# Kernel optimization log

Hardware: AMD Instinct MI355X
Metric: run time of the kernel (lower is better)

Reference implementation:

```python
import jax, jax.numpy as jnp
import numpy as np

B, T, D, E, C = 4, 4096, 2048, 8, 1024
H = D // E  # per-expert hidden = out_features // num_experts = 256


def setup_inputs() -> dict:
    key = jax.random.key(0)
    ks = jax.random.split(key, 7)
    x = jax.random.normal(ks[0], (B, T, D), dtype=jnp.float32)
    # nn.Linear-style init scale ~ 1/sqrt(fan_in)
    W1 = jax.random.normal(ks[1], (E, H, D), dtype=jnp.float32) / np.sqrt(D)
    b1 = jax.random.normal(ks[2], (E, H), dtype=jnp.float32) / np.sqrt(D)
    W2 = jax.random.normal(ks[3], (E, D, H), dtype=jnp.float32) / np.sqrt(D)
    b2 = jax.random.normal(ks[4], (D,), dtype=jnp.float32) / np.sqrt(D)
    expert_indices = jax.random.randint(ks[5], (B, E, C), 0, T, dtype=jnp.int32)
    expert_gate = jax.random.uniform(ks[6], (B, E, C), dtype=jnp.float32)
    return {"x": x, "W1": W1, "b1": b1, "W2": W2, "b2": b2,
            "expert_indices": expert_indices, "expert_gate": expert_gate,
            "num_tokens": T}


def reference(x, W1, b1, W2, b2, expert_indices, expert_gate, num_tokens):
    # x: (B,T,D); expert_indices/expert_gate: (B,E,C)
    Bb = x.shape[0]
    Ee, Cc = expert_indices.shape[1], expert_indices.shape[2]
    b_idx = jnp.arange(Bb)[:, None, None]
    # dispatch: gather tokens per expert -> (B,E,C,D)
    sel = x[b_idx, expert_indices]
    # contract: per-expert GEMM -> (B,E,C,H)
    h = jnp.einsum('becd,ehd->bech', sel, W1) + b1[None, :, None, :]
    h = jax.nn.gelu(h, approximate=False)
    # expand: per-expert GEMM -> (B,E,C,D), shared output bias
    y = jnp.einsum('bech,eoh->beco', h, W2) + b2
    y = y * expert_gate[..., None]
    # combine: gated scatter-add back to token positions -> (B,T,D)
    out = jnp.zeros((Bb, num_tokens, x.shape[2]), dtype=x.dtype)
    out = out.at[jnp.arange(Bb)[:, None], expert_indices.reshape(Bb, Ee * Cc)].add(
        y.reshape(Bb, Ee * Cc, -1))
    return out
```

## Files before the change

### kernel.cpp

```cpp
#include <hip/hip_runtime.h>
#include <hip/hip_bf16.h>
#include <math.h>

#define B_ 4
#define T_ 4096
#define D_ 2048
#define E_ 8
#define C_ 1024
#define H_ 256
#define SLOTCAP 32

typedef unsigned short u16;
typedef unsigned long long u64;
typedef __attribute__((ext_vector_type(8))) short short8;
typedef __attribute__((ext_vector_type(4))) float f32x4;

__device__ __forceinline__ u16 f2bf_n(float f) {
    union { __hip_bfloat16 b; u16 u; } v;
    v.b = __float2bfloat16(f);
    return v.u;
}
__device__ __forceinline__ float bf2f(u16 u) {
    union { unsigned u; float f; } v; v.u = ((unsigned)u) << 16;
    return v.f;
}

__device__ __forceinline__ int swz(int row, int chunk) {
    return (row << 6) + ((chunk ^ (row & 7)) << 3);
}

__device__ __forceinline__ void gload16(const void* g, void* l) {
    __builtin_amdgcn_global_load_lds(
        (const __attribute__((address_space(1))) void*)g,
        (__attribute__((address_space(3))) void*)l, 16, 0, 0);
}

__global__ __launch_bounds__(256) void conv_x_bf16(
    const float* __restrict__ src, u16* __restrict__ dst, int n)
{
    int i = (blockIdx.x * 256 + threadIdx.x) * 4;
    if (i >= n) return;
    f32x4 v = *reinterpret_cast<const f32x4*>(src + i);
    u16 o[4];
    o[0] = f2bf_n(v[0]); o[1] = f2bf_n(v[1]); o[2] = f2bf_n(v[2]); o[3] = f2bf_n(v[3]);
    *reinterpret_cast<u64*>(dst + i) = *reinterpret_cast<const u64*>(o);
}

__global__ __launch_bounds__(256) void conv_w1_img(
    const float* __restrict__ W1, u16* __restrict__ img)
{
    const int cid = blockIdx.x * 256 + threadIdx.x;
    const int e = cid >> 16;
    const int kt = (cid >> 11) & 31;
    const int row = (cid >> 3) & 255;
    const int sc = cid & 7;
    const float* s = W1 + (((size_t)e * 256 + row) * 2048 + kt * 64
                           + ((sc ^ (row & 7)) << 3));
    f32x4 v0 = *reinterpret_cast<const f32x4*>(s);
    f32x4 v1 = *reinterpret_cast<const f32x4*>(s + 4);
    u16 o[8];
    #pragma unroll
    for (int j = 0; j < 4; ++j) { o[j] = f2bf_n(v0[j]); o[j + 4] = f2bf_n(v1[j]); }
    *reinterpret_cast<short8*>(img + (size_t)cid * 8) =
        *reinterpret_cast<const short8*>(o);
}

__global__ __launch_bounds__(256) void conv_w2_img(
    const float* __restrict__ W2, u16* __restrict__ img)
{
    const int cid = blockIdx.x * 256 + threadIdx.x;
    const int e = cid >> 16;
    const int nt = (cid >> 13) & 7;
    const int kt = (cid >> 11) & 3;
    const int row = (cid >> 3) & 255;
    const int sc = cid & 7;
    const float* s = W2 + (((size_t)e * 2048 + nt * 256 + row) * 256 + kt * 64
                           + ((sc ^ (row & 7)) << 3));
    f32x4 v0 = *reinterpret_cast<const f32x4*>(s);
    f32x4 v1 = *reinterpret_cast<const f32x4*>(s + 4);
    u16 o[8];
    #pragma unroll
    for (int j = 0; j < 4; ++j) { o[j] = f2bf_n(v0[j]); o[j + 4] = f2bf_n(v1[j]); }
    *reinterpret_cast<short8*>(img + (size_t)cid * 8) =
        *reinterpret_cast<const short8*>(o);
}

__global__ __launch_bounds__(512) void gemm1_v8(
    const u16* __restrict__ xbf, const u16* __restrict__ W1img,
    const float* __restrict__ b1, const int* __restrict__ idx,
    u16* __restrict__ Himg)
{
    const int be = blockIdx.x;
    const int mt = blockIdx.y;
    const int b = be >> 3, e = be & 7;
    const int m0 = mt * 64;

    __shared__ __align__(16) u16 As[2][4096];
    __shared__ __align__(16) u16 Bs[2][16384];

    const int tid = threadIdx.x;
    const int lane = tid & 63, wid = tid >> 6;
    const int wm = wid >> 2, wn = wid & 3;
    const int l15 = lane & 15, lk = lane >> 4;

    const int row8 = tid >> 3, asc = tid & 7;
    const int tok = idx[(b * E_ + e) * C_ + m0 + row8];
    const u16* aSrc = xbf + ((size_t)b * T_ + tok) * D_
                          + ((asc ^ (row8 & 7)) << 3);
    const u16* bSrc = W1img + (size_t)e * 32 * 16384 + (size_t)tid * 8;
    const int wofs = wid * 512;

#define G1_ISSUE(buf, t)                                                      \
    do {                                                                      \
        gload16(aSrc + (t) * 64, &As[buf][wofs]);                             \
        const u16* b_ = bSrc + (size_t)(t) * 16384;                           \
        gload16(b_,         &Bs[buf][wofs]);                                  \
        gload16(b_ + 4096,  &Bs[buf][4096 + wofs]);                           \
        gload16(b_ + 8192,  &Bs[buf][8192 + wofs]);                           \
        gload16(b_ + 12288, &Bs[buf][12288 + wofs]);                          \
    } while (0)

    f32x4 acc[2][4];
    #pragma unroll
    for (int i = 0; i < 2; ++i)
        #pragma unroll
        for (int j = 0; j < 4; ++j)
            acc[i][j] = (f32x4){0.f, 0.f, 0.f, 0.f};

    G1_ISSUE(0, 0);
    G1_ISSUE(1, 1);

    const int NT = D_ / 64;
    for (int t = 0; t < NT; ++t) {
        const int cur = t & 1;
        if (t < NT - 1) asm volatile("s_waitcnt vmcnt(5)" ::: "memory");
        else            asm volatile("s_waitcnt vmcnt(0)" ::: "memory");
        __builtin_amdgcn_s_barrier();
        __builtin_amdgcn_sched_barrier(0);
        #pragma unroll
        for (int kk = 0; kk < 2; ++kk) {
            short8 af[2], bfr[4];
            #pragma unroll
            for (int m = 0; m < 2; ++m) {
                const int row = wm * 32 + m * 16 + l15;
                af[m] = *reinterpret_cast<const short8*>(
                    &As[cur][swz(row, kk * 4 + lk)]);
            }
            #pragma unroll
            for (int n = 0; n < 4; ++n) {
                const int row = wn * 64 + n * 16 + l15;
                bfr[n] = *reinterpret_cast<const short8*>(
                    &Bs[cur][swz(row, kk * 4 + lk)]);
            }
            __builtin_amdgcn_s_setprio(1);
            #pragma unroll
            for (int m = 0; m < 2; ++m)
                #pragma unroll
                for (int n = 0; n < 4; ++n)
                    acc[m][n] = __builtin_amdgcn_mfma_f32_16x16x32_bf16(
                        bfr[n], af[m], acc[m][n], 0, 0, 0);
            __builtin_amdgcn_s_setprio(0);
        }
        asm volatile("s_waitcnt lgkmcnt(0)" ::: "memory");
        __builtin_amdgcn_s_barrier();
        __builtin_amdgcn_sched_barrier(0);
        if (t + 2 < NT) G1_ISSUE(cur, t + 2);
    }
#undef G1_ISSUE

    const size_t hblk = ((size_t)(be * 16 + mt) * 4 + wn) * 4096;
    #pragma unroll
    for (int m = 0; m < 2; ++m) {
        const int row = wm * 32 + m * 16 + l15;
        #pragma unroll
        for (int n = 0; n < 4; ++n) {
            const int hb = wn * 64 + n * 16 + lk * 4;
            f32x4 bias = *reinterpret_cast<const f32x4*>(&b1[e * H_ + hb]);
            u16 o[4];
            #pragma unroll
            for (int r = 0; r < 4; ++r) {
                float h = acc[m][n][r] + bias[r];
                float g = 0.5f * h * (1.0f + erff(h * 0.70710678118f));
                o[r] = f2bf_n(g);
            }
            const int lc = (n * 2 + (lk >> 1)) ^ (row & 7);
            u16* p = Himg + hblk + row * 64 + lc * 8 + (lk & 1) * 4;
            *reinterpret_cast<u64*>(p) = *reinterpret_cast<const u64*>(o);
        }
    }
}

__global__ __launch_bounds__(512) void gemm2_v6(
    const u16* __restrict__ Himg, const u16* __restrict__ W2img,
    const float* __restrict__ b2, const float* __restrict__ gate,
    u16* __restrict__ Ybuf)
{
    const int be = blockIdx.x;
    const int yy = blockIdx.y;
    const int mt = yy >> 3, nt = yy & 7;
    const int b = be >> 3, e = be & 7;
    const int m0 = mt * 64, n0 = nt * 256;

    __shared__ __align__(16) u16 As[2][4096];
    __shared__ __align__(16) u16 Bs[2][16384];

    const int tid = threadIdx.x;
    const int lane = tid & 63, wid = tid >> 6;
    const int wm = wid >> 2, wn = wid & 3;
    const int l15 = lane & 15, lk = lane >> 4;

    const u16* aSrc = Himg + ((size_t)(be * 16 + mt) * 4) * 4096 + (size_t)tid * 8;
    const u16* bSrc = W2img + ((size_t)(e * 8 + nt) * 4) * 16384 + (size_t)tid * 8;
    const int wofs = wid * 512;

#define G2_ISSUE(buf, t)                                                      \
    do {                                                                      \
        gload16(aSrc + (size_t)(t) * 4096, &As[buf][wofs]);                   \
        const u16* b_ = bSrc + (size_t)(t) * 16384;                           \
        gload16(b_,         &Bs[buf][wofs]);                                  \
        gload16(b_ + 4096,  &Bs[buf][4096 + wofs]);                           \
        gload16(b_ + 8192,  &Bs[buf][8192 + wofs]);                           \
        gload16(b_ + 12288, &Bs[buf][12288 + wofs]);                          \
    } while (0)

    f32x4 acc[2][4];
    #pragma unroll
    for (int i = 0; i < 2; ++i)
        #pragma unroll
        for (int j = 0; j < 4; ++j)
            acc[i][j] = (f32x4){0.f, 0.f, 0.f, 0.f};

    G2_ISSUE(0, 0);
    G2_ISSUE(1, 1);

    const int NT = H_ / 64;
    for (int t = 0; t < NT; ++t) {
        const int cur = t & 1;
        if (t < NT - 1) asm volatile("s_waitcnt vmcnt(5)" ::: "memory");
        else            asm volatile("s_waitcnt vmcnt(0)" ::: "memory");
        __builtin_amdgcn_s_barrier();
        __builtin_amdgcn_sched_barrier(0);
        #pragma unroll
        for (int kk = 0; kk < 2; ++kk) {
            short8 af[2], bfr[4];
            #pragma unroll
            for (int m = 0; m < 2; ++m) {
                const int row = wm * 32 + m * 16 + l15;
                af[m] = *reinterpret_cast<const short8*>(
                    &As[cur][swz(row, kk * 4 + lk)]);
            }
            #pragma unroll
            for (int n = 0; n < 4; ++n) {
                const int row = wn * 64 + n * 16 + l15;
                bfr[n] = *reinterpret_cast<const short8*>(
                    &Bs[cur][swz(row, kk * 4 + lk)]);
            }
            __builtin_amdgcn_s_setprio(1);
            #pragma unroll
            for (int m = 0; m < 2; ++m)
                #pragma unroll
                for (int n = 0; n < 4; ++n)
                    acc[m][n] = __builtin_amdgcn_mfma_f32_16x16x32_bf16(
                        bfr[n], af[m], acc[m][n], 0, 0, 0);
            __builtin_amdgcn_s_setprio(0);
        }
        asm volatile("s_waitcnt lgkmcnt(0)" ::: "memory");
        __builtin_amdgcn_s_barrier();
        __builtin_amdgcn_sched_barrier(0);
        if (t + 2 < NT) G2_ISSUE(cur, t + 2);
    }
#undef G2_ISSUE

    const size_t ybase = (size_t)(b * E_ + e) * C_ + m0;
    #pragma unroll
    for (int m = 0; m < 2; ++m) {
        const int cl = wm * 32 + m * 16 + l15;
        const float g = gate[ybase + cl];
        u16* rowp = Ybuf + (ybase + cl) * (size_t)D_ + n0;
        #pragma unroll
        for (int n = 0; n < 4; ++n) {
            const int db = wn * 64 + n * 16 + lk * 4;
            f32x4 bias = *reinterpret_cast<const f32x4*>(&b2[n0 + db]);
            u16 o[4];
            #pragma unroll
            for (int r = 0; r < 4; ++r)
                o[r] = f2bf_n((acc[m][n][r] + bias[r]) * g);
            *reinterpret_cast<u64*>(rowp + db) = *reinterpret_cast<const u64*>(o);
        }
    }
}

__global__ __launch_bounds__(256) void fill_kernel(
    const int* __restrict__ idx, int* __restrict__ cnt,
    int* __restrict__ slots)
{
    int i = blockIdx.x * 256 + threadIdx.x;
    if (i >= B_ * E_ * C_) return;
    int b = i / (E_ * C_);
    int slot = i % (E_ * C_);
    int t = idx[i];
    int p = atomicAdd(&cnt[b * T_ + t], 1);
    if (p < SLOTCAP) slots[(b * T_ + t) * SLOTCAP + p] = slot;
}

__global__ __launch_bounds__(256) void combine_kernel(
    const u16* __restrict__ Ybuf, const int* __restrict__ cnt,
    const int* __restrict__ slots, float* __restrict__ out)
{
    const int bt = blockIdx.x;
    const int tid = threadIdx.x;
    __shared__ int sl[SLOTCAP];
    int n = cnt[bt];
    n = n > SLOTCAP ? SLOTCAP : n;
    if (tid < n) sl[tid] = slots[bt * SLOTCAP + tid];
    __syncthreads();
    const int b = bt >> 12;
    float a[8] = {0.f, 0.f, 0.f, 0.f, 0.f, 0.f, 0.f, 0.f};
    for (int s = 0; s < n; ++s) {
        const u16* yrow = Ybuf + ((size_t)b * (E_ * C_) + sl[s]) * D_ + tid * 8;
        short8 v = *reinterpret_cast<const short8*>(yrow);
        #pragma unroll
        for (int j = 0; j < 8; ++j) a[j] += bf2f((u16)v[j]);
    }
    float* orow = out + (size_t)bt * D_ + tid * 8;
    *reinterpret_cast<f32x4*>(orow)     = (f32x4){a[0], a[1], a[2], a[3]};
    *reinterpret_cast<f32x4*>(orow + 4) = (f32x4){a[4], a[5], a[6], a[7]};
}

extern "C" void kernel_launch(void* const* d_in, const int* in_sizes, int n_in,
                              void* d_out, int out_size, void* d_ws, size_t ws_size,
                              hipStream_t stream) {
    const float* x    = (const float*)d_in[0];
    const float* W1   = (const float*)d_in[1];
    const float* b1   = (const float*)d_in[2];
    const float* W2   = (const float*)d_in[3];
    const float* b2   = (const float*)d_in[4];
    const int*   idx  = (const int*)d_in[5];
    const float* gate = (const float*)d_in[6];
    float* out = (float*)d_out;

    const size_t nW = (size_t)E_ * H_ * D_;
    const size_t nX = (size_t)B_ * T_ * D_;
    const size_t nH = (size_t)B_ * E_ * C_ * H_;
    const size_t nY = (size_t)B_ * E_ * C_ * D_;

    u16* W1img = (u16*)d_ws;
    u16* W2img = W1img + nW;
    u16* Himg  = W2img + nW;
    u16* Ybuf  = Himg + nH;
    u16* xbf   = Ybuf;
    int* cnt   = (int*)(Ybuf + nY);
    int* slots = cnt + (size_t)B_ * T_;

    hipMemsetAsync(cnt, 0, (size_t)B_ * T_ * sizeof(int), stream);
    conv_w1_img<<<2048, 256, 0, stream>>>(W1, W1img);
    conv_w2_img<<<2048, 256, 0, stream>>>(W2, W2img);
    conv_x_bf16<<<(int)(nX / 1024), 256, 0, stream>>>(x, xbf, (int)nX);
    fill_kernel<<<(B_ * E_ * C_) / 256, 256, 0, stream>>>(idx, cnt, slots);

    gemm1_v8<<<dim3(32, 16), 512, 0, stream>>>(xbf, W1img, b1, idx, Himg);
    gemm2_v6<<<dim3(32, 128), 512, 0, stream>>>(Himg, W2img, b2, gate, Ybuf);
    combine_kernel<<<B_ * T_, 256, 0, stream>>>(Ybuf, cnt, slots, out);
}
```

Baseline: 223.9 us.

## Keep whole W2 panel resident in LDS and loop over M tiles per block

The second GEMM now loads the full 256x256 W2 panel for its expert/N-tile into shared memory once, then iterates over all 16 M tiles of H within one block, prefetching the next A tile during the epilogue. This removes the repeated reload of W2 tiles across 16 separate blocks and cuts the grid from 4096 to 256 blocks. In exchange it uses about 160KB of LDS per block, leaving one block per CU with single-buffered A, and the grid is 256 blocks, so latency hiding and parallelism are reduced.

```diff
diff --git a/kernel.cpp b/kernel.cpp
--- a/kernel.cpp
+++ b/kernel.cpp
@@ -190,104 +190,124 @@
     }
 }
 
-__global__ __launch_bounds__(512) void gemm2_v6(
+__global__ __launch_bounds__(512) void gemm2_v7(
     const u16* __restrict__ Himg, const u16* __restrict__ W2img,
     const float* __restrict__ b2, const float* __restrict__ gate,
     u16* __restrict__ Ybuf)
 {
     const int be = blockIdx.x;
-    const int yy = blockIdx.y;
-    const int mt = yy >> 3, nt = yy & 7;
+    const int nt = blockIdx.y;
     const int b = be >> 3, e = be & 7;
-    const int m0 = mt * 64, n0 = nt * 256;
-
-    __shared__ __align__(16) u16 As[2][4096];
-    __shared__ __align__(16) u16 Bs[2][16384];
+    const int n0 = nt * 256;
+
+    __shared__ __align__(16) u16 As[16384];
+    __shared__ __align__(16) u16 Bs[65536];
 
     const int tid = threadIdx.x;
     const int lane = tid & 63, wid = tid >> 6;
     const int wm = wid >> 2, wn = wid & 3;
     const int l15 = lane & 15, lk = lane >> 4;
-
-    const u16* aSrc = Himg + ((size_t)(be * 16 + mt) * 4) * 4096 + (size_t)tid * 8;
-    const u16* bSrc = W2img + ((size_t)(e * 8 + nt) * 4) * 16384 + (size_t)tid * 8;
     const int wofs = wid * 512;
 
-#define G2_ISSUE(buf, t)                                                      \
+    const u16* bPanel = W2img + (size_t)(e * 8 + nt) * 65536;
+    #pragma unroll
+    for (int j = 0; j < 16; ++j)
+        gload16(bPanel + (size_t)(j * 512 + tid) * 8, &Bs[j * 4096 + wofs]);
+
+    const u16* aBase = Himg + (size_t)(be * 16) * 16384 + (size_t)tid * 8;
+
+#define A_ISSUE(mt)                                                           \
     do {                                                                      \
-        gload16(aSrc + (size_t)(t) * 4096, &As[buf][wofs]);                   \
-        const u16* b_ = bSrc + (size_t)(t) * 16384;                           \
-        gload16(b_,         &Bs[buf][wofs]);                                  \
-        gload16(b_ + 4096,  &Bs[buf][4096 + wofs]);                           \
-        gload16(b_ + 8192,  &Bs[buf][8192 + wofs]);                           \
-        gload16(b_ + 12288, &Bs[buf][12288 + wofs]);                          \
+        const u16* a_ = aBase + (size_t)(mt) * 16384;                         \
+        gload16(a_,          &As[wofs]);                                      \
+        gload16(a_ + 4096,   &As[4096 + wofs]);                               \
+        gload16(a_ + 8192,   &As[8192 + wofs]);                               \
+        gload16(a_ + 12288,  &As[12288 + wofs]);                              \
     } while (0)
 
-    f32x4 acc[2][4];
-    #pragma unroll
-    for (int i = 0; i < 2; ++i)
-        #pragma unroll
-        for (int j = 0; j < 4; ++j)
-            acc[i][j] = (f32x4){0.f, 0.f, 0.f, 0.f};
-
-    G2_ISSUE(0, 0);
-    G2_ISSUE(1, 1);
-
-    const int NT = H_ / 64;
-    for (int t = 0; t < NT; ++t) {
-        const int cur = t & 1;
-        if (t < NT - 1) asm volatile("s_waitcnt vmcnt(5)" ::: "memory");
-        else            asm volatile("s_waitcnt vmcnt(0)" ::: "memory");
-        __builtin_amdgcn_s_barrier();
-        __builtin_amdgcn_sched_barrier(0);
-        #pragma unroll
-        for (int kk = 0; kk < 2; ++kk) {
-            short8 af[2], bfr[4];
-            #pragma unroll
-            for (int m = 0; m < 2; ++m) {
-                const int row = wm * 32 + m * 16 + l15;
-                af[m] = *reinterpret_cast<const short8*>(
-                    &As[cur][swz(row, kk * 4 + lk)]);
-            }
-            #pragma unroll
-            for (int n = 0; n < 4; ++n) {
-                const int row = wn * 64 + n * 16 + l15;
-                bfr[n] = *reinterpret_cast<const short8*>(
-                    &Bs[cur][swz(row, kk * 4 + lk)]);
-            }
-            __builtin_amdgcn_s_setprio(1);
-            #pragma unroll
-            for (int m = 0; m < 2; ++m)
-                #pragma unroll
-                for (int n = 0; n < 4; ++n)
-                    acc[m][n] = __builtin_amdgcn_mfma_f32_16x16x32_bf16(
-                        bfr[n], af[m], acc[m][n], 0, 0, 0);
-            __builtin_amdgcn_s_setprio(0);
-        }
+    A_ISSUE(0);
+
+    f32x4 bias[4];
+    #pragma unroll
+    for (int n = 0; n < 4; ++n)
+        bias[n] = *reinterpret_cast<const f32x4*>(
+            &b2[n0 + wn * 64 + n * 16 + lk * 4]);
+
+    const int gbase = (b * E_ + e) * C_;
+    const size_t ybase = (size_t)(b * E_ + e) * C_;
+
+    asm volatile("s_waitcnt vmcnt(0)" ::: "memory");
+    __builtin_amdgcn_s_barrier();
+    __builtin_amdgcn_sched_barrier(0);
+
+    for (int mt = 0; mt < 16; ++mt) {
+        f32x4 acc[2][4];
+        #pragma unroll
+        for (int i = 0; i < 2; ++i)
+            #pragma unroll
+            for (int j = 0; j < 4; ++j)
+                acc[i][j] = (f32x4){0.f, 0.f, 0.f, 0.f};
+
+        #pragma unroll
+        for (int t = 0; t < 4; ++t) {
+            #pragma unroll
+            for (int kk = 0; kk < 2; ++kk) {
+                short8 af[2], bfr[4];
+                #pragma unroll
+                for (int m = 0; m < 2; ++m) {
+                    const int row = wm * 32 + m * 16 + l15;
+                    af[m] = *reinterpret_cast<const short8*>(
+                        &As[t * 4096 + swz(row, kk * 4 + lk)]);
+                }
+                #pragma unroll
+                for (int n = 0; n < 4; ++n) {
+                    const int row = wn * 64 + n * 16 + l15;
+                    bfr[n] = *reinterpret_cast<const short8*>(
+                        &Bs[t * 16384 + swz(row, kk * 4 + lk)]);
+                }
+                __builtin_amdgcn_s_setprio(1);
+                #pragma unroll
+                for (int m = 0; m < 2; ++m)
+                    #pragma unroll
+                    for (int n = 0; n < 4; ++n)
+                        acc[m][n] = __builtin_amdgcn_mfma_f32_16x16x32_bf16(
+                            bfr[n], af[m], acc[m][n], 0, 0, 0);
+                __builtin_amdgcn_s_setprio(0);
+            }
+        }
+
         asm volatile("s_waitcnt lgkmcnt(0)" ::: "memory");
         __builtin_amdgcn_s_barrier();
         __builtin_amdgcn_sched_barrier(0);
-        if (t + 2 < NT) G2_ISSUE(cur, t + 2);
+
+        const float g0 = gate[gbase + mt * 64 + wm * 32 + l15];
+        const float g1 = gate[gbase + mt * 64 + wm * 32 + 16 + l15];
+        if (mt < 15) A_ISSUE(mt + 1);
+
+        #pragma unroll
+        for (int m = 0; m < 2; ++m) {
+            const int cl = wm * 32 + m * 16 + l15;
+            const float g = (m == 0) ? g0 : g1;
+            u16* rowp = Ybuf + (ybase + mt * 64 + cl) * (size_t)D_ + n0;
+            #pragma unroll
+            for (int n = 0; n < 4; ++n) {
+                const int db = wn * 64 + n * 16 + lk * 4;
+                u16 o[4];
+                #pragma unroll
+                for (int r = 0; r < 4; ++r)
+                    o[r] = f2bf_n((acc[m][n][r] + bias[n][r]) * g);
+                *reinterpret_cast<u64*>(rowp + db) =
+                    *reinterpret_cast<const u64*>(o);
+            }
+        }
+
+        if (mt < 15) {
+            asm volatile("s_waitcnt vmcnt(8)" ::: "memory");
+            __builtin_amdgcn_s_barrier();
+            __builtin_amdgcn_sched_barrier(0);
+        }
     }
-#undef G2_ISSUE
-
-    const size_t ybase = (size_t)(b * E_ + e) * C_ + m0;
-    #pragma unroll
-    for (int m = 0; m < 2; ++m) {
-        const int cl = wm * 32 + m * 16 + l15;
-        const float g = gate[ybase + cl];
-        u16* rowp = Ybuf + (ybase + cl) * (size_t)D_ + n0;
-        #pragma unroll
-        for (int n = 0; n < 4; ++n) {
-            const int db = wn * 64 + n * 16 + lk * 4;
-            f32x4 bias = *reinterpret_cast<const f32x4*>(&b2[n0 + db]);
-            u16 o[4];
-            #pragma unroll
-            for (int r = 0; r < 4; ++r)
-                o[r] = f2bf_n((acc[m][n][r] + bias[r]) * g);
-            *reinterpret_cast<u64*>(rowp + db) = *reinterpret_cast<const u64*>(o);
-        }
-    }
+#undef A_ISSUE
 }
 
 __global__ __launch_bounds__(256) void fill_kernel(
@@ -359,6 +379,6 @@
     fill_kernel<<<(B_ * E_ * C_) / 256, 256, 0, stream>>>(idx, cnt, slots);
 
     gemm1_v8<<<dim3(32, 16), 512, 0, stream>>>(xbf, W1img, b1, idx, Himg);
-    gemm2_v6<<<dim3(32, 128), 512, 0, stream>>>(Himg, W2img, b2, gate, Ybuf);
+    gemm2_v7<<<dim3(32, 8), 512, 0, stream>>>(Himg, W2img, b2, gate, Ybuf);
     combine_kernel<<<B_ * T_, 256, 0, stream>>>(Ybuf, cnt, slots, out);
 }
```

Result: faster. 218.3 us (-2.5%).
